# Kernel optimization log

Measured on AMD Instinct MI355X. Metric: run time of the kernel, lower is better.

The kernel has to match this reference:

```python
import jax, jax.numpy as jnp
import numpy as np
from jax import lax

VOCAB = 2048
HID = 1024
BATCH = 64
SEQ = 256

def setup_inputs() -> dict:
    key = jax.random.key(0)
    ks = jax.random.split(key, 6)
    s = 0.02
    return {
        "X": jax.random.randint(ks[0], (BATCH, SEQ), 0, VOCAB),
        # gate weights stacked as [f, i, o, c_tilde] along output dim (same math as 4 separate Linears)
        "W1": jax.random.normal(ks[1], (VOCAB + HID, 4 * HID), jnp.float32) * s,
        "b1": jnp.zeros((4 * HID,), jnp.float32),
        "W2": jax.random.normal(ks[2], (HID + HID, 4 * HID), jnp.float32) * s,
        "b2": jnp.zeros((4 * HID,), jnp.float32),
        "W3": jax.random.normal(ks[3], (HID + HID, 4 * HID), jnp.float32) * s,
        "b3": jnp.zeros((4 * HID,), jnp.float32),
        "Wout": jax.random.normal(ks[4], (HID, VOCAB), jnp.float32) * s,
        "bout": jnp.zeros((VOCAB,), jnp.float32),
    }

def _cell(x, h, c, W, b):
    # concat(x, h) @ [Wf|Wi|Wo|Wc] + b -> split into 4 gates
    g = jnp.concatenate([x, h], axis=1) @ W + b
    f, i, o, ct = jnp.split(g, 4, axis=1)
    c = jax.nn.sigmoid(f) * c + jax.nn.sigmoid(i) * jnp.tanh(ct)
    h = jax.nn.sigmoid(o) * jnp.tanh(c)
    return h, c

def reference(X, W1, b1, W2, b2, W3, b3, Wout, bout):
    Xoh = jax.nn.one_hot(X.T, VOCAB, dtype=jnp.float32)  # [T, B, V]
    z = jnp.zeros((BATCH, HID), jnp.float32)
    init = (z, z, z, z, z, z)

    def step(carry, x):
        h1, c1, h2, c2, h3, c3 = carry
        h1, c1 = _cell(x, h1, c1, W1, b1)
        h2, c2 = _cell(h1, h2, c2, W2, b2)
        h3, c3 = _cell(h2, h3, c3, W3, b3)
        y = h3 @ Wout + bout  # [B, V]
        return (h1, c1, h2, c2, h3, c3), y

    carry, ys = lax.scan(step, init, Xoh)
    out = ys.reshape(SEQ * BATCH, VOCAB)  # == torch.cat(outputs, dim=0)
    h1, c1, h2, c2, h3, c3 = carry
    return (out, h1, c1, h2, c2, h3, c3)
```

## Files before the change

kernel.cpp:

```cpp
#include <hip/hip_runtime.h>
#include <hip/hip_cooperative_groups.h>
#include <math.h>

namespace cg = cooperative_groups;

#define NBLK 256
#define NTHR 512
#define HID  1024
#define NB   64
#define SEQL 256
#define VOC  2048
#define G4   4096

typedef __attribute__((ext_vector_type(8))) short bf16x8;
typedef __attribute__((ext_vector_type(4))) float f32x4;

#define STG_STRIDE 520

struct SmemT {
    short stg_hi[16 * STG_STRIDE];
    short stg_lo[16 * STG_STRIDE];
    f32x4 red[8][64];
    float tile[64 * 17];
    float cst[3 * 4 * 64];
    int   tok[64];
};

__device__ __forceinline__ float sigm(float x) { return 1.0f / (1.0f + expf(-x)); }

template<int KTOT, int MTILES>
__device__ void run_gemm(SmemT* sm, const float* __restrict__ W, int ldw, int wrow0,
                         const short* __restrict__ Ahi0, const short* __restrict__ Alo0,
                         const short* __restrict__ Ahi1, const short* __restrict__ Alo1,
                         bool gatecols, int cb, int mbase)
{
    constexpr int WPM = 8 / MTILES;
    constexpr int RPW = 512 / WPM;
    constexpr int KS  = RPW / 32;
    constexpr int NCH = KTOT / 512;

    const int tid = threadIdx.x;
    const int l   = tid & 63, w = tid >> 6;
    const int c16 = l & 15,  g = l >> 4;
    const int mt  = w / WPM, sub = w % WPM;
    const int sg  = tid & 3, kp  = tid >> 2;
    const int gc  = gatecols ? (sg * HID + cb) : (cb + sg * 4);

    f32x4 acc = {0.f, 0.f, 0.f, 0.f};

    for (int ch = 0; ch < NCH; ++ch) {
        #pragma unroll
        for (int rep = 0; rep < 2; ++rep) {
            const int kpair = kp + rep * 128;
            const int row   = wrow0 + ch * 512 + kpair * 2;
            const float4 w0 = *(const float4*)(W + (size_t)row * ldw + gc);
            const float4 w1 = *(const float4*)(W + (size_t)(row + 1) * ldw + gc);
            const float* a = (const float*)&w0;
            const float* b = (const float*)&w1;
            #pragma unroll
            for (int c = 0; c < 4; ++c) {
                const uint32_t ua = __float_as_uint(a[c]);
                const uint32_t ub = __float_as_uint(b[c]);
                const uint32_t hi = (ub & 0xFFFF0000u) | (ua >> 16);
                const float la = a[c] - __uint_as_float(ua & 0xFFFF0000u);
                const float lb = b[c] - __uint_as_float(ub & 0xFFFF0000u);
                const uint32_t lo = (__float_as_uint(lb) & 0xFFFF0000u)
                                  | (__float_as_uint(la) >> 16);
                const int off = (sg * 4 + c) * STG_STRIDE + kpair * 2;
                *(uint32_t*)&sm->stg_hi[off] = hi;
                *(uint32_t*)&sm->stg_lo[off] = lo;
            }
        }
        __syncthreads();

        const int kglob0 = ch * 512;
        const short* ahi = (KTOT == 2048 && kglob0 >= 1024) ? Ahi1 : Ahi0;
        const short* alo = (KTOT == 2048 && kglob0 >= 1024) ? Alo1 : Alo0;
        const int kk0 = kglob0 & 1023;
        const size_t arow = (size_t)(mbase + mt * 16 + c16) * HID;
        const short* ah = ahi + arow + kk0 + sub * RPW + g * 8;
        const short* al = alo + arow + kk0 + sub * RPW + g * 8;
        const short* bh = sm->stg_hi + c16 * STG_STRIDE + sub * RPW + g * 8;
        const short* bl = sm->stg_lo + c16 * STG_STRIDE + sub * RPW + g * 8;
        #pragma unroll
        for (int ks = 0; ks < KS; ++ks) {
            const bf16x8 a_hi = *(const bf16x8*)(ah + ks * 32);
            const bf16x8 a_lo = *(const bf16x8*)(al + ks * 32);
            const bf16x8 b_hi = *(const bf16x8*)(bh + ks * 32);
            const bf16x8 b_lo = *(const bf16x8*)(bl + ks * 32);
            acc = __builtin_amdgcn_mfma_f32_16x16x32_bf16(a_hi, b_hi, acc, 0, 0, 0);
            acc = __builtin_amdgcn_mfma_f32_16x16x32_bf16(a_lo, b_hi, acc, 0, 0, 0);
            acc = __builtin_amdgcn_mfma_f32_16x16x32_bf16(a_hi, b_lo, acc, 0, 0, 0);
        }
        __syncthreads();
    }

    sm->red[w][l] = acc;
    __syncthreads();
    if (sub == 0) {
        #pragma unroll
        for (int j = 1; j < WPM; ++j) {
            const f32x4 o = sm->red[w + j][l];
            acc[0] += o[0]; acc[1] += o[1]; acc[2] += o[2]; acc[3] += o[3];
        }
        const int r0 = mt * 16 + (l >> 4) * 4;
        sm->tile[(r0 + 0) * 17 + c16] = acc[0];
        sm->tile[(r0 + 1) * 17 + c16] = acc[1];
        sm->tile[(r0 + 2) * 17 + c16] = acc[2];
        sm->tile[(r0 + 3) * 17 + c16] = acc[3];
    }
    __syncthreads();
}

__device__ void gate_epilogue(SmemT* sm, int layer, const float* __restrict__ bias,
                              const float* __restrict__ W1gather, int hjb,
                              short* __restrict__ Hhi, short* __restrict__ Hlo)
{
    const int tid = threadIdx.x;
    if (tid < 256) {
        const int m = tid & 63, dh = tid >> 6;
        float f  = sm->tile[m * 17 + dh]       + bias[hjb + dh];
        float i  = sm->tile[m * 17 + 4 + dh]   + bias[HID + hjb + dh];
        float o  = sm->tile[m * 17 + 8 + dh]   + bias[2 * HID + hjb + dh];
        float ct = sm->tile[m * 17 + 12 + dh]  + bias[3 * HID + hjb + dh];
        if (W1gather) {
            const float* wr = W1gather + (size_t)sm->tok[m] * G4 + hjb + dh;
            f += wr[0]; i += wr[HID]; o += wr[2 * HID]; ct += wr[3 * HID];
        }
        const int ci = (layer * 4 + dh) * 64 + m;
        const float cn = sigm(f) * sm->cst[ci] + sigm(i) * tanhf(ct);
        sm->cst[ci] = cn;
        const float h = sigm(o) * tanhf(cn);
        const uint32_t uh = __float_as_uint(h);
        const float hiF = __uint_as_float(uh & 0xFFFF0000u);
        const float loV = h - hiF;
        const size_t idx = (size_t)m * HID + hjb + dh;
        Hhi[idx] = (short)(uh >> 16);
        Hlo[idx] = (short)(__float_as_uint(loV) >> 16);
    }
}

__device__ void y_epilogue(SmemT* sm, int t, const float* __restrict__ bo,
                           int vc0, int mh, float* __restrict__ out)
{
    const int tid = threadIdx.x;
    const int mloc = tid >> 4, c = tid & 15;
    const float v = sm->tile[mloc * 17 + c] + bo[vc0 + c];
    const int m = mh * 32 + mloc;
    __builtin_nontemporal_store(v, out + ((size_t)t * NB + m) * VOC + vc0 + c);
}

__global__ __launch_bounds__(NTHR, 1) void lstm3_mfma(
    const int*   __restrict__ X,
    const float* __restrict__ W1, const float* __restrict__ b1,
    const float* __restrict__ W2, const float* __restrict__ b2,
    const float* __restrict__ W3, const float* __restrict__ b3,
    const float* __restrict__ Wo, const float* __restrict__ bo,
    float* __restrict__ out, short* __restrict__ hws)
{
    cg::grid_group grid = cg::this_grid();
    __shared__ SmemT sm;

    const int tid = threadIdx.x;
    const int blk = blockIdx.x;
    const int tile = (blk & 7) * 32 + (blk >> 3);
    const int hjb  = tile * 4;
    const int q    = blk >> 3;
    const int ytile = (blk & 7) * 16 + (q & 15);
    const int mh    = q >> 4;
    const int vc0   = ytile * 16;

    uint32_t* wz = (uint32_t*)hws;
    for (int i = blk * NTHR + tid; i < 6 * 65536; i += NBLK * NTHR) wz[i] = 0u;
    for (int i = tid; i < 768; i += NTHR) sm.cst[i] = 0.f;
    grid.sync();

    #define HHI(l_, s_) (hws + ((l_) * 2 + (s_)) * 131072)
    #define HLO(l_, s_) (hws + ((l_) * 2 + (s_)) * 131072 + 65536)

    for (int s = 0; s <= SEQL + 2; ++s) {
        if (s < SEQL && tid < 64) sm.tok[tid] = X[tid * SEQL + s];

        if (s < SEQL) {
            const int t = s, sl = t & 1, sp = sl ^ 1;
            run_gemm<1024, 4>(&sm, W1, G4, VOC, HHI(0, sp), HLO(0, sp),
                              nullptr, nullptr, true, hjb, 0);
            gate_epilogue(&sm, 0, b1, W1, hjb, HHI(0, sl), HLO(0, sl));
        }
        if (s >= 1 && s <= SEQL) {
            const int t = s - 1, sl = t & 1, sp = sl ^ 1;
            run_gemm<2048, 4>(&sm, W2, G4, 0, HHI(0, sl), HLO(0, sl),
                              HHI(1, sp), HLO(1, sp), true, hjb, 0);
            gate_epilogue(&sm, 1, b2, nullptr, hjb, HHI(1, sl), HLO(1, sl));
        }
        if (s >= 2 && s <= SEQL + 1) {
            const int t = s - 2, sl = t & 1, sp = sl ^ 1;
            run_gemm<2048, 4>(&sm, W3, G4, 0, HHI(1, sl), HLO(1, sl),
                              HHI(2, sp), HLO(2, sp), true, hjb, 0);
            gate_epilogue(&sm, 2, b3, nullptr, hjb, HHI(2, sl), HLO(2, sl));
        }
        if (s >= 3) {
            const int t = s - 3, sl = t & 1;
            run_gemm<1024, 2>(&sm, Wo, VOC, 0, HHI(2, sl), HLO(2, sl),
                              nullptr, nullptr, false, vc0, mh * 32);
            y_epilogue(&sm, t, bo, vc0, mh, out);
        }
        grid.sync();
    }

    if (tid < 256) {
        const int m = tid & 63, dh = tid >> 6;
        const size_t base = (size_t)SEQL * NB * VOC;
        #pragma unroll
        for (int lyr = 0; lyr < 3; ++lyr) {
            const short* hh = HHI(lyr, 1);
            const short* hl = HLO(lyr, 1);
            const size_t idx = (size_t)m * HID + hjb + dh;
            const float h = __uint_as_float(((uint32_t)(uint16_t)hh[idx]) << 16)
                          + __uint_as_float(((uint32_t)(uint16_t)hl[idx]) << 16);
            out[base + (size_t)(2 * lyr) * 65536 + idx] = h;
            out[base + (size_t)(2 * lyr + 1) * 65536 + idx] =
                sm.cst[(lyr * 4 + dh) * 64 + m];
        }
    }
}

extern "C" void kernel_launch(void* const* d_in, const int* in_sizes, int n_in,
                              void* d_out, int out_size, void* d_ws, size_t ws_size,
                              hipStream_t stream)
{
    const int*   X  = (const int*)  d_in[0];
    const float* W1 = (const float*)d_in[1];
    const float* b1 = (const float*)d_in[2];
    const float* W2 = (const float*)d_in[3];
    const float* b2 = (const float*)d_in[4];
    const float* W3 = (const float*)d_in[5];
    const float* b3 = (const float*)d_in[6];
    const float* Wo = (const float*)d_in[7];
    const float* bo = (const float*)d_in[8];
    float* out = (float*)d_out;
    short* hws = (short*)d_ws;

    void* args[] = { &X, &W1, &b1, &W2, &b2, &W3, &b3, &Wo, &bo, &out, &hws };
    hipLaunchCooperativeKernel((const void*)lstm3_mfma,
                               dim3(NBLK), dim3(NTHR), args, 0, stream);
}
```

Before: 25.35 ms.

## Prepack weights into swizzled bf16 hi/lo images and split layers across block groups

Adds a new cooperative kernel that first converts each block's weight slices into pre-split bf16 hi/lo, LDS-swizzled images in workspace. It then streams those images through a double-buffered LDS pipeline instead of converting fp32 weights on every timestep. The layers are also split across two groups of 128 blocks (layer1+layer3 versus layer2+output projection), so each block does less work per step and the wider tiles change the parallel decomposition. The cost is a large workspace requirement and a one-time pack pass per call, with a fallback to the old kernel when the workspace is too small.

```diff
diff --git a/kernel.cpp b/kernel.cpp
--- a/kernel.cpp
+++ b/kernel.cpp
@@ -15,9 +15,330 @@
 typedef __attribute__((ext_vector_type(8))) short bf16x8;
 typedef __attribute__((ext_vector_type(4))) float f32x4;
 
+__device__ __forceinline__ float sigm(float x) { return 1.0f / (1.0f + expf(-x)); }
+
+#define OFF_P1 0u
+#define OFF_P2 16777216u
+#define OFF_P3 50331648u
+#define OFF_PY 83886080u
+#define OFF_H  92274688u
+#define OFF_C  93847552u
+#define WS_NEED 94633984ull
+
+struct SmemF {
+    short bbuf[2][32768];
+    float tile[64 * 33];
+    f32x4 red[8][64];
+    int   tok[64];
+};
+
+__device__ void prepack_gate(uint32_t* __restrict__ img, const float* __restrict__ W,
+                             int row0, int ta)
+{
+    for (int s = threadIdx.x; s < 16384; s += NTHR) {
+        const int b4 = s * 4;
+        const int plane = b4 >> 15;
+        const int bb = b4 & 32767;
+        const int L = bb >> 10;
+        const int r = (bb & 1023) ^ ((L & 7) << 4);
+        const int k = r >> 1;
+        const int col = (L >> 3) * 1024 + ta * 8 + (L & 7);
+        const float v0 = W[(size_t)(row0 + k) * G4 + col];
+        const float v1 = W[(size_t)(row0 + k + 1) * G4 + col];
+        uint32_t u;
+        if (plane == 0) {
+            u = (__float_as_uint(v0) >> 16) | (__float_as_uint(v1) & 0xFFFF0000u);
+        } else {
+            const float l0 = v0 - __uint_as_float(__float_as_uint(v0) & 0xFFFF0000u);
+            const float l1 = v1 - __uint_as_float(__float_as_uint(v1) & 0xFFFF0000u);
+            u = (__float_as_uint(l0) >> 16) | (__float_as_uint(l1) & 0xFFFF0000u);
+        }
+        img[s] = u;
+    }
+}
+
+__device__ void prepack_y(uint32_t* __restrict__ img, const float* __restrict__ Wo,
+                          int row0, int ty)
+{
+    for (int s = threadIdx.x; s < 8192; s += NTHR) {
+        const int b4 = s * 4;
+        const int plane = b4 >> 14;
+        const int bb = b4 & 16383;
+        const int L = bb >> 10;
+        const int r = (bb & 1023) ^ ((L & 7) << 4);
+        const int k = r >> 1;
+        const int col = ty * 16 + L;
+        const float v0 = Wo[(size_t)(row0 + k) * VOC + col];
+        const float v1 = Wo[(size_t)(row0 + k + 1) * VOC + col];
+        uint32_t u;
+        if (plane == 0) {
+            u = (__float_as_uint(v0) >> 16) | (__float_as_uint(v1) & 0xFFFF0000u);
+        } else {
+            const float l0 = v0 - __uint_as_float(__float_as_uint(v0) & 0xFFFF0000u);
+            const float l1 = v1 - __uint_as_float(__float_as_uint(v1) & 0xFFFF0000u);
+            u = (__float_as_uint(l0) >> 16) | (__float_as_uint(l1) & 0xFFFF0000u);
+        }
+        img[s] = u;
+    }
+}
+
+template<int NCH, bool TWOSEG>
+__device__ __forceinline__ void gemm_gate(SmemF* sm, const char* __restrict__ pack,
+    const short* __restrict__ A0, const short* __restrict__ A1)
+{
+    const int tid = threadIdx.x;
+    const int w = tid >> 6, lane = tid & 63;
+    const int mt = w >> 1, nt = w & 1;
+    const int c16 = lane & 15, g = lane >> 4;
+    const int Lcol = nt * 16 + c16;
+    const int swz = (Lcol & 7) << 4;
+
+    f32x4 acc = {0.f, 0.f, 0.f, 0.f};
+    uint4 st[8];
+
+    #pragma unroll
+    for (int i = 0; i < 8; ++i)
+        st[i] = *(const uint4*)(pack + (i * NTHR + tid) * 16);
+    #pragma unroll
+    for (int i = 0; i < 8; ++i)
+        *(uint4*)((char*)sm->bbuf[0] + (i * NTHR + tid) * 16) = st[i];
+    __syncthreads();
+
+    #pragma unroll
+    for (int ch = 0; ch < NCH; ++ch) {
+        if (ch + 1 < NCH) {
+            const char* src = pack + (size_t)(ch + 1) * 65536;
+            #pragma unroll
+            for (int i = 0; i < 8; ++i)
+                st[i] = *(const uint4*)(src + (i * NTHR + tid) * 16);
+        }
+        const short* Aseg = (TWOSEG && ch >= 2) ? A1 : A0;
+        const int kk0 = (TWOSEG ? (ch & 1) : ch) * 512;
+        const short* ah = Aseg + (size_t)(mt * 16 + c16) * 1024 + kk0 + g * 8;
+        const short* al = ah + 65536;
+        const char* bb = (const char*)sm->bbuf[ch & 1];
+        #pragma unroll
+        for (int ks = 0; ks < 16; ++ks) {
+            const int bofs = (Lcol * 1024 + ks * 64 + g * 16) ^ swz;
+            const bf16x8 b_h = *(const bf16x8*)(bb + bofs);
+            const bf16x8 b_l = *(const bf16x8*)(bb + 32768 + bofs);
+            const bf16x8 a_h = *(const bf16x8*)(ah + ks * 32);
+            const bf16x8 a_l = *(const bf16x8*)(al + ks * 32);
+            acc = __builtin_amdgcn_mfma_f32_16x16x32_bf16(a_h, b_h, acc, 0, 0, 0);
+            acc = __builtin_amdgcn_mfma_f32_16x16x32_bf16(a_l, b_h, acc, 0, 0, 0);
+            acc = __builtin_amdgcn_mfma_f32_16x16x32_bf16(a_h, b_l, acc, 0, 0, 0);
+        }
+        if (ch + 1 < NCH) {
+            #pragma unroll
+            for (int i = 0; i < 8; ++i)
+                *(uint4*)((char*)sm->bbuf[(ch + 1) & 1] + (i * NTHR + tid) * 16) = st[i];
+        }
+        __syncthreads();
+    }
+    const int r0 = mt * 16 + g * 4;
+    sm->tile[(r0 + 0) * 33 + Lcol] = acc[0];
+    sm->tile[(r0 + 1) * 33 + Lcol] = acc[1];
+    sm->tile[(r0 + 2) * 33 + Lcol] = acc[2];
+    sm->tile[(r0 + 3) * 33 + Lcol] = acc[3];
+    __syncthreads();
+}
+
+__device__ __forceinline__ void gemm_y(SmemF* sm, const char* __restrict__ pack,
+                                       const short* __restrict__ A0)
+{
+    const int tid = threadIdx.x;
+    const int w = tid >> 6, lane = tid & 63;
+    const int mt = w >> 1, kh = w & 1;
+    const int c16 = lane & 15, g = lane >> 4;
+    const int swz = (c16 & 7) << 4;
+
+    f32x4 acc = {0.f, 0.f, 0.f, 0.f};
+    uint4 st[4];
+    #pragma unroll
+    for (int i = 0; i < 4; ++i)
+        st[i] = *(const uint4*)(pack + (i * NTHR + tid) * 16);
+    #pragma unroll
+    for (int i = 0; i < 4; ++i)
+        *(uint4*)((char*)sm->bbuf[0] + (i * NTHR + tid) * 16) = st[i];
+    __syncthreads();
+
+    #pragma unroll
+    for (int ch = 0; ch < 2; ++ch) {
+        if (ch == 0) {
+            const char* src = pack + 32768;
+            #pragma unroll
+            for (int i = 0; i < 4; ++i)
+                st[i] = *(const uint4*)(src + (i * NTHR + tid) * 16);
+        }
+        const int kk0 = ch * 512 + kh * 256;
+        const short* ah = A0 + (size_t)(mt * 16 + c16) * 1024 + kk0 + g * 8;
+        const short* al = ah + 65536;
+        const char* bb = (const char*)sm->bbuf[ch & 1];
+        #pragma unroll
+        for (int ks = 0; ks < 8; ++ks) {
+            const int koff = kh * 256 + ks * 32 + g * 8;
+            const int bofs = (c16 * 1024 + koff * 2) ^ swz;
+            const bf16x8 b_h = *(const bf16x8*)(bb + bofs);
+            const bf16x8 b_l = *(const bf16x8*)(bb + 16384 + bofs);
+            const bf16x8 a_h = *(const bf16x8*)(ah + ks * 32);
+            const bf16x8 a_l = *(const bf16x8*)(al + ks * 32);
+            acc = __builtin_amdgcn_mfma_f32_16x16x32_bf16(a_h, b_h, acc, 0, 0, 0);
+            acc = __builtin_amdgcn_mfma_f32_16x16x32_bf16(a_l, b_h, acc, 0, 0, 0);
+            acc = __builtin_amdgcn_mfma_f32_16x16x32_bf16(a_h, b_l, acc, 0, 0, 0);
+        }
+        if (ch == 0) {
+            #pragma unroll
+            for (int i = 0; i < 4; ++i)
+                *(uint4*)((char*)sm->bbuf[1] + (i * NTHR + tid) * 16) = st[i];
+        }
+        __syncthreads();
+    }
+    sm->red[w][lane] = acc;
+    __syncthreads();
+}
+
+__device__ __forceinline__ void gate_epi(SmemF* sm, const float* __restrict__ bias,
+    const float* __restrict__ Wgather, float* __restrict__ cst,
+    short* __restrict__ Hout, int ta)
+{
+    const int tid = threadIdx.x;
+    const int m = tid & 63, u = tid >> 6;
+    const int hb = ta * 8 + u;
+    const float* tl = sm->tile + m * 33;
+    float f  = tl[u]      + bias[hb];
+    float i  = tl[8 + u]  + bias[1024 + hb];
+    float o  = tl[16 + u] + bias[2048 + hb];
+    float ct = tl[24 + u] + bias[3072 + hb];
+    if (Wgather) {
+        const float* wr = Wgather + (size_t)sm->tok[m] * G4 + hb;
+        f += wr[0]; i += wr[1024]; o += wr[2048]; ct += wr[3072];
+    }
+    float* cp = cst + hb * 64 + m;
+    const float cn = sigm(f) * (*cp) + sigm(i) * tanhf(ct);
+    *cp = cn;
+    const float h = sigm(o) * tanhf(cn);
+    const uint32_t uh = __float_as_uint(h);
+    const float lof = h - __uint_as_float(uh & 0xFFFF0000u);
+    Hout[m * 1024 + hb] = (short)(uh >> 16);
+    Hout[65536 + m * 1024 + hb] = (short)(__float_as_uint(lof) >> 16);
+}
+
+__device__ __forceinline__ void y_epi(SmemF* sm, int t, const float* __restrict__ bo,
+                                      int vc0, float* __restrict__ out)
+{
+    const int tid = threadIdx.x;
+    const int c = tid & 15, m0 = tid >> 4;
+    #pragma unroll
+    for (int hh = 0; hh < 2; ++hh) {
+        const int m = m0 + hh * 32;
+        const int mt = m >> 4, mr = m & 15;
+        const int l = ((mr >> 2) << 4) | c;
+        const int i = mr & 3;
+        const float v = sm->red[mt * 2][l][i] + sm->red[mt * 2 + 1][l][i] + bo[vc0 + c];
+        __builtin_nontemporal_store(v, out + ((size_t)t * NB + m) * VOC + vc0 + c);
+    }
+    __syncthreads();
+}
+
+__device__ __forceinline__ float recon(const short* __restrict__ Hp, size_t idx)
+{
+    return __uint_as_float(((uint32_t)(uint16_t)Hp[idx]) << 16)
+         + __uint_as_float(((uint32_t)(uint16_t)Hp[65536 + idx]) << 16);
+}
+
+__global__ __launch_bounds__(NTHR, 2) void lstm3_v3(
+    const int*   __restrict__ X,
+    const float* __restrict__ W1, const float* __restrict__ b1,
+    const float* __restrict__ W2, const float* __restrict__ b2,
+    const float* __restrict__ W3, const float* __restrict__ b3,
+    const float* __restrict__ Wo, const float* __restrict__ bo,
+    float* __restrict__ out, char* __restrict__ wsb)
+{
+    cg::grid_group grid = cg::this_grid();
+    __shared__ SmemF sm;
+
+    const int tid = threadIdx.x, blk = blockIdx.x;
+    const bool grpA = blk < 128;
+    const int bb_ = grpA ? blk : blk - 128;
+    const int ta = (bb_ & 7) * 16 + (bb_ >> 3);
+
+    uint32_t* zr = (uint32_t*)(wsb + OFF_H);
+    for (int i = blk * NTHR + tid; i < 589824; i += NBLK * NTHR) zr[i] = 0u;
+
+    if (grpA) {
+        for (int ch = 0; ch < 2; ++ch)
+            prepack_gate((uint32_t*)(wsb + OFF_P1 + (size_t)ta * 131072 + ch * 65536),
+                         W1, VOC + ch * 512, ta);
+        for (int ch = 0; ch < 4; ++ch)
+            prepack_gate((uint32_t*)(wsb + OFF_P3 + (size_t)ta * 262144 + ch * 65536),
+                         W3, ch * 512, ta);
+    } else {
+        for (int ch = 0; ch < 4; ++ch)
+            prepack_gate((uint32_t*)(wsb + OFF_P2 + (size_t)ta * 262144 + ch * 65536),
+                         W2, ch * 512, ta);
+        for (int ch = 0; ch < 2; ++ch)
+            prepack_y((uint32_t*)(wsb + OFF_PY + (size_t)ta * 65536 + ch * 32768),
+                      Wo, ch * 512, ta);
+    }
+    grid.sync();
+
+    short* H = (short*)(wsb + OFF_H);
+    float* C = (float*)(wsb + OFF_C);
+    #define HP(l_, s_) (H + ((l_) * 2 + (s_)) * 131072)
+
+    for (int s = 0; s <= SEQL + 2; ++s) {
+        if (tid < 64 && s < SEQL) sm.tok[tid] = X[tid * SEQL + s];
+
+        if (grpA) {
+            if (s < SEQL) {
+                const int sl = s & 1;
+                gemm_gate<2, false>(&sm, wsb + OFF_P1 + (size_t)ta * 131072,
+                                    HP(0, sl ^ 1), nullptr);
+                gate_epi(&sm, b1, W1, C + 0 * 65536, HP(0, sl), ta);
+            }
+            if (s >= 2 && s <= SEQL + 1) {
+                const int t = s - 2, sl = t & 1;
+                gemm_gate<4, true>(&sm, wsb + OFF_P3 + (size_t)ta * 262144,
+                                   HP(1, sl), HP(2, sl ^ 1));
+                gate_epi(&sm, b3, nullptr, C + 2 * 65536, HP(2, sl), ta);
+            }
+        } else {
+            if (s >= 1 && s <= SEQL) {
+                const int t = s - 1, sl = t & 1;
+                gemm_gate<4, true>(&sm, wsb + OFF_P2 + (size_t)ta * 262144,
+                                   HP(0, sl), HP(1, sl ^ 1));
+                gate_epi(&sm, b2, nullptr, C + 1 * 65536, HP(1, sl), ta);
+            }
+            if (s >= 3) {
+                const int t = s - 3, sl = t & 1;
+                gemm_y(&sm, wsb + OFF_PY + (size_t)ta * 65536, HP(2, sl));
+                y_epi(&sm, t, bo, ta * 16, out);
+            }
+        }
+        grid.sync();
+    }
+
+    {
+        const int m = tid & 63, u = tid >> 6;
+        const size_t base = (size_t)SEQL * NB * VOC;
+        const size_t idx = (size_t)m * 1024 + ta * 8 + u;
+        const int cu = (ta * 8 + u) * 64 + m;
+        if (grpA) {
+            out[base + idx]               = recon(HP(0, 1), idx);
+            out[base + 65536 + idx]       = C[0 * 65536 + cu];
+            out[base + 4 * 65536 + idx]   = recon(HP(2, 1), idx);
+            out[base + 5 * 65536 + idx]   = C[2 * 65536 + cu];
+        } else {
+            out[base + 2 * 65536 + idx]   = recon(HP(1, 1), idx);
+            out[base + 3 * 65536 + idx]   = C[1 * 65536 + cu];
+        }
+    }
+    #undef HP
+}
+
 #define STG_STRIDE 520
 
-struct SmemT {
+struct SmemFB {
     short stg_hi[16 * STG_STRIDE];
     short stg_lo[16 * STG_STRIDE];
     f32x4 red[8][64];
@@ -26,13 +347,11 @@
     int   tok[64];
 };
 
-__device__ __forceinline__ float sigm(float x) { return 1.0f / (1.0f + expf(-x)); }
-
 template<int KTOT, int MTILES>
-__device__ void run_gemm(SmemT* sm, const float* __restrict__ W, int ldw, int wrow0,
-                         const short* __restrict__ Ahi0, const short* __restrict__ Alo0,
-                         const short* __restrict__ Ahi1, const short* __restrict__ Alo1,
-                         bool gatecols, int cb, int mbase)
+__device__ void fb_gemm(SmemFB* sm, const float* __restrict__ W, int ldw, int wrow0,
+                        const short* __restrict__ Ahi0, const short* __restrict__ Alo0,
+                        const short* __restrict__ Ahi1, const short* __restrict__ Alo1,
+                        bool gatecols, int cb, int mbase)
 {
     constexpr int WPM = 8 / MTILES;
     constexpr int RPW = 512 / WPM;
@@ -112,9 +431,9 @@
     __syncthreads();
 }
 
-__device__ void gate_epilogue(SmemT* sm, int layer, const float* __restrict__ bias,
-                              const float* __restrict__ W1gather, int hjb,
-                              short* __restrict__ Hhi, short* __restrict__ Hlo)
+__device__ void fb_gate_epi(SmemFB* sm, int layer, const float* __restrict__ bias,
+                            const float* __restrict__ W1gather, int hjb,
+                            short* __restrict__ Hhi, short* __restrict__ Hlo)
 {
     const int tid = threadIdx.x;
     if (tid < 256) {
@@ -140,8 +459,8 @@
     }
 }
 
-__device__ void y_epilogue(SmemT* sm, int t, const float* __restrict__ bo,
-                           int vc0, int mh, float* __restrict__ out)
+__device__ void fb_y_epi(SmemFB* sm, int t, const float* __restrict__ bo,
+                         int vc0, int mh, float* __restrict__ out)
 {
     const int tid = threadIdx.x;
     const int mloc = tid >> 4, c = tid & 15;
@@ -150,7 +469,7 @@
     __builtin_nontemporal_store(v, out + ((size_t)t * NB + m) * VOC + vc0 + c);
 }
 
-__global__ __launch_bounds__(NTHR, 1) void lstm3_mfma(
+__global__ __launch_bounds__(NTHR, 1) void lstm3_fb(
     const int*   __restrict__ X,
     const float* __restrict__ W1, const float* __restrict__ b1,
     const float* __restrict__ W2, const float* __restrict__ b2,
@@ -159,7 +478,7 @@
     float* __restrict__ out, short* __restrict__ hws)
 {
     cg::grid_group grid = cg::this_grid();
-    __shared__ SmemT sm;
+    __shared__ SmemFB sm;
 
     const int tid = threadIdx.x;
     const int blk = blockIdx.x;
@@ -183,27 +502,27 @@
 
         if (s < SEQL) {
             const int t = s, sl = t & 1, sp = sl ^ 1;
-            run_gemm<1024, 4>(&sm, W1, G4, VOC, HHI(0, sp), HLO(0, sp),
-                              nullptr, nullptr, true, hjb, 0);
-            gate_epilogue(&sm, 0, b1, W1, hjb, HHI(0, sl), HLO(0, sl));
+            fb_gemm<1024, 4>(&sm, W1, G4, VOC, HHI(0, sp), HLO(0, sp),
+                             nullptr, nullptr, true, hjb, 0);
+            fb_gate_epi(&sm, 0, b1, W1, hjb, HHI(0, sl), HLO(0, sl));
         }
         if (s >= 1 && s <= SEQL) {
             const int t = s - 1, sl = t & 1, sp = sl ^ 1;
-            run_gemm<2048, 4>(&sm, W2, G4, 0, HHI(0, sl), HLO(0, sl),
-                              HHI(1, sp), HLO(1, sp), true, hjb, 0);
-            gate_epilogue(&sm, 1, b2, nullptr, hjb, HHI(1, sl), HLO(1, sl));
+            fb_gemm<2048, 4>(&sm, W2, G4, 0, HHI(0, sl), HLO(0, sl),
+                             HHI(1, sp), HLO(1, sp), true, hjb, 0);
+            fb_gate_epi(&sm, 1, b2, nullptr, hjb, HHI(1, sl), HLO(1, sl));
         }
         if (s >= 2 && s <= SEQL + 1) {
             const int t = s - 2, sl = t & 1, sp = sl ^ 1;
-            run_gemm<2048, 4>(&sm, W3, G4, 0, HHI(1, sl), HLO(1, sl),
-                              HHI(2, sp), HLO(2, sp), true, hjb, 0);
-            gate_epilogue(&sm, 2, b3, nullptr, hjb, HHI(2, sl), HLO(2, sl));
+            fb_gemm<2048, 4>(&sm, W3, G4, 0, HHI(1, sl), HLO(1, sl),
+                             HHI(2, sp), HLO(2, sp), true, hjb, 0);
+            fb_gate_epi(&sm, 2, b3, nullptr, hjb, HHI(2, sl), HLO(2, sl));
         }
         if (s >= 3) {
             const int t = s - 3, sl = t & 1;
-            run_gemm<1024, 2>(&sm, Wo, VOC, 0, HHI(2, sl), HLO(2, sl),
-                              nullptr, nullptr, false, vc0, mh * 32);
-            y_epilogue(&sm, t, bo, vc0, mh, out);
+            fb_gemm<1024, 2>(&sm, Wo, VOC, 0, HHI(2, sl), HLO(2, sl),
+                             nullptr, nullptr, false, vc0, mh * 32);
+            fb_y_epi(&sm, t, bo, vc0, mh, out);
         }
         grid.sync();
     }
@@ -223,6 +542,8 @@
                 sm.cst[(lyr * 4 + dh) * 64 + m];
         }
     }
+    #undef HHI
+    #undef HLO
 }
 
 extern "C" void kernel_launch(void* const* d_in, const int* in_sizes, int n_in,
@@ -239,9 +560,16 @@
     const float* Wo = (const float*)d_in[7];
     const float* bo = (const float*)d_in[8];
     float* out = (float*)d_out;
-    short* hws = (short*)d_ws;
-
-    void* args[] = { &X, &W1, &b1, &W2, &b2, &W3, &b3, &Wo, &bo, &out, &hws };
-    hipLaunchCooperativeKernel((const void*)lstm3_mfma,
-                               dim3(NBLK), dim3(NTHR), args, 0, stream);
-}
+
+    if (ws_size >= WS_NEED) {
+        char* wsb = (char*)d_ws;
+        void* args[] = { &X, &W1, &b1, &W2, &b2, &W3, &b3, &Wo, &bo, &out, &wsb };
+        hipLaunchCooperativeKernel((const void*)lstm3_v3,
+                                   dim3(NBLK), dim3(NTHR), args, 0, stream);
+    } else {
+        short* hws = (short*)d_ws;
+        void* args[] = { &X, &W1, &b1, &W2, &b2, &W3, &b3, &Wo, &bo, &out, &hws };
+        hipLaunchCooperativeKernel((const void*)lstm3_fb,
+                                   dim3(NBLK), dim3(NTHR), args, 0, stream);
+    }
+}
```

Measured after the change: 24.07 ms. 5.1% less time.
